# Optimization experiments

Measured on AMD Instinct MI355X. Metric: run time of the kernel, lower is better.

The kernel has to match this reference:

```python
import jax, jax.numpy as jnp
import numpy as np

B, M, T, N = 128, 256, 512, 512

def setup_inputs() -> dict:
    key = jax.random.key(0)
    ks = jax.random.split(key, 6)
    return {
        "hidden_state": jax.random.normal(ks[0], (B, M), jnp.float32),
        "cell_state": jax.random.normal(ks[1], (B, M), jnp.float32),
        "X": jax.random.normal(ks[2], (B, T, N), jnp.float32),
        "We1": jax.random.normal(ks[3], (2 * M, T), jnp.float32) * 0.05,
        "be1": jnp.zeros((T,), jnp.float32),
        "We2": jax.random.normal(ks[4], (T, T), jnp.float32) * 0.05,
        "be2": jnp.zeros((T,), jnp.float32),
        "v": jax.random.normal(ks[5], (T, 1), jnp.float32) * 0.05,
        "bv": jnp.zeros((1,), jnp.float32),
    }

def reference(hidden_state, cell_state, X, We1, be1, We2, be2, v, bv):
    # concat hidden + cell: [B, 2m]; Dense(T) then broadcast over n (K.repeat)
    hc = jnp.concatenate([hidden_state, cell_state], axis=-1)
    hs = (hc @ We1 + be1)[:, None, :]                 # [B, 1, T] (broadcast over n)
    # Permute X -> [B, n, T], Dense(T): contract over T
    ux = jnp.einsum('btn,tk->bnk', X, We2) + be2      # [B, n, T]
    # add + tanh + Dense(1) fused chain
    e = jnp.tanh(hs + ux) @ v + bv                    # [B, n, 1]
    # Permute -> [B, 1, n], softmax over last axis (n)
    attn = jax.nn.softmax(jnp.swapaxes(e, 1, 2), axis=-1)  # [B, 1, n]
    return attn
```

## Files before the change

kernel.cpp:

```cpp
#include <hip/hip_runtime.h>
#include <hip/hip_bf16.h>


typedef _Float16 half8 __attribute__((ext_vector_type(8)));
typedef float floatx4 __attribute__((ext_vector_type(4)));

__device__ __forceinline__ float fast_tanh(float x) {
    float cx = fminf(15.0f, fmaxf(-15.0f, x));
    float e = __expf(2.0f * cx);
    return (e - 1.0f) * __fdividef(1.0f, e + 1.0f);
}

__global__ __launch_bounds__(256) void k_prep_b(const float* __restrict__ We2,
                                                _Float16* __restrict__ Bf) {
    __shared__ float tl[64][133];
    const int kblk = blockIdx.x >> 3, ts = blockIdx.x & 7;
    const int k0 = kblk << 7, t0 = ts << 6;
    for (int idx = threadIdx.x; idx < 64 * 128; idx += 256) {
        int tr = idx >> 7, kc = idx & 127;
        tl[tr][kc] = We2[(t0 + tr) * 512 + k0 + kc];
    }
    __syncthreads();
    _Float16* dst = Bf + (size_t)(kblk * 8 + ts) * 8192;
#pragma unroll
    for (int i = 0; i < 4; ++i) {
        int s  = threadIdx.x + (i << 8);
        int h  = s >> 9, c = (s >> 6) & 7, ln = s & 63;
        int kl = c * 16 + (ln & 15);
        int tb = h * 32 + (ln >> 4) * 8;
        half8 hh;
#pragma unroll
        for (int j = 0; j < 8; ++j) hh[j] = (_Float16)tl[tb + j][kl];
        *(half8*)&dst[s * 8] = hh;
    }
}

__global__ __launch_bounds__(256) void k_hs(const float* __restrict__ hidden,
                                            const float* __restrict__ cell,
                                            const float* __restrict__ We1,
                                            const float* __restrict__ be1,
                                            const float* __restrict__ be2,
                                            float* __restrict__ g) {
    __shared__ __align__(16) float hcl[8][512];
    __shared__ float red[4][8][64];
    const int b0 = (blockIdx.x >> 3) << 3;
    const int k0 = (blockIdx.x & 7) << 6;
    for (int idx = threadIdx.x; idx < 8 * 512; idx += 256) {
        int bi = idx >> 9, j = idx & 511;
        hcl[bi][j] = (j < 256) ? hidden[(b0 + bi) * 256 + j]
                               : cell[(b0 + bi) * 256 + j - 256];
    }
    __syncthreads();
    const int kl = threadIdx.x & 63;
    const int jc = threadIdx.x >> 6;
    const int k  = k0 + kl;
    float acc[8] = {};
    for (int j = jc * 128; j < jc * 128 + 128; j += 4) {
        float w0 = We1[(j + 0) * 512 + k];
        float w1 = We1[(j + 1) * 512 + k];
        float w2 = We1[(j + 2) * 512 + k];
        float w3 = We1[(j + 3) * 512 + k];
#pragma unroll
        for (int bi = 0; bi < 8; ++bi) {
            float4 h = *(const float4*)&hcl[bi][j];
            acc[bi] += h.x * w0 + h.y * w1 + h.z * w2 + h.w * w3;
        }
    }
#pragma unroll
    for (int bi = 0; bi < 8; ++bi) red[jc][bi][kl] = acc[bi];
    __syncthreads();
    for (int idx = threadIdx.x; idx < 512; idx += 256) {
        int bi = idx >> 6, kk = idx & 63;
        float s = red[0][bi][kk] + red[1][bi][kk] + red[2][bi][kk] + red[3][bi][kk];
        int kg = k0 + kk;
        g[(b0 + bi) * 512 + kg] = s + be1[kg] + be2[kg];
    }
}

__global__ __launch_bounds__(256, 3) void k_main(const float* __restrict__ X,
                                                 const _Float16* __restrict__ Bf,
                                                 const float* __restrict__ g,
                                                 const float* __restrict__ vvec,
                                                 float* __restrict__ Ep) {
    __shared__ __align__(16) _Float16 Xs[2][8192];
    const int tid  = threadIdx.x;
    const int lane = tid & 63;
    const int wv   = tid >> 6;
    const int l16  = lane & 15;
    const int lhi  = lane >> 4;
    const int logical = ((blockIdx.x & 7) << 8) | (blockIdx.x >> 3);
    const int mt   = logical >> 2;
    const int kblk = logical & 3;
    const int b    = mt >> 2;
    const int n0   = (mt & 3) << 7;
    const int mw   = wv >> 1;
    const int kw   = wv & 1;

    const float* Xg = X + (size_t)b * 262144 + n0;
    int sm[4], st[4], su[4];
#pragma unroll
    for (int i = 0; i < 4; ++i) {
        int s  = tid + (i << 8);
        int m  = s & 127, lh = (s >> 7) & 3, h = s >> 9;
        sm[i] = m;
        st[i] = h * 32 + lh * 8;
        su[i] = ((h * 8 + (m >> 4)) * 64 + lh * 16 + (m & 15)) * 8;
    }
    const _Float16* Bw = Bf + (size_t)kblk * 65536 + (size_t)kw * 2048 +
                         (size_t)lane * 8;

    float xr[32];
#pragma unroll
    for (int i = 0; i < 4; ++i)
#pragma unroll
        for (int j = 0; j < 8; ++j)
            xr[i * 8 + j] = Xg[(size_t)(st[i] + j) * 512 + sm[i]];
#pragma unroll
    for (int i = 0; i < 4; ++i) {
        half8 hh;
#pragma unroll
        for (int j = 0; j < 8; ++j) hh[j] = (_Float16)xr[i * 8 + j];
        *(half8*)&Xs[0][su[i]] = hh;
    }
    __syncthreads();

    floatx4 acc[4][4];
#pragma unroll
    for (int a = 0; a < 4; ++a)
#pragma unroll
        for (int c = 0; c < 4; ++c) acc[a][c] = (floatx4){0.f, 0.f, 0.f, 0.f};

#pragma unroll
    for (int ts = 0; ts < 8; ++ts) {
        const int cur = ts & 1, nxt = cur ^ 1;
        if (ts < 7) {
#pragma unroll
            for (int i = 0; i < 4; ++i)
#pragma unroll
                for (int j = 0; j < 8; ++j)
                    xr[i * 8 + j] =
                        Xg[(size_t)((ts + 1) * 64 + st[i] + j) * 512 + sm[i]];
        }
        __builtin_amdgcn_sched_barrier(0);
#pragma unroll
        for (int h = 0; h < 2; ++h) {
            half8 af[4], bf[4];
#pragma unroll
            for (int mf = 0; mf < 4; ++mf)
                af[mf] = *(const half8*)
                    &Xs[cur][((h * 8 + mw * 4 + mf) * 64 + lane) * 8];
#pragma unroll
            for (int nf = 0; nf < 4; ++nf)
                bf[nf] = *(const half8*)
                    (Bw + (size_t)ts * 8192 + h * 4096 + nf * 512);
#pragma unroll
            for (int mf = 0; mf < 4; ++mf)
#pragma unroll
                for (int nf = 0; nf < 4; ++nf)
                    acc[mf][nf] = __builtin_amdgcn_mfma_f32_16x16x32_f16(
                        af[mf], bf[nf], acc[mf][nf], 0, 0, 0);
        }
        if (ts < 7) {
#pragma unroll
            for (int i = 0; i < 4; ++i) {
                half8 hh;
#pragma unroll
                for (int j = 0; j < 8; ++j) hh[j] = (_Float16)xr[i * 8 + j];
                *(half8*)&Xs[nxt][su[i]] = hh;
            }
        }
        __syncthreads();
    }

    const float* gb = g + b * 512 + kblk * 128;
    const float* vb = vvec + kblk * 128;
    float sl[4][4];
#pragma unroll
    for (int mf = 0; mf < 4; ++mf)
#pragma unroll
        for (int r = 0; r < 4; ++r) sl[mf][r] = 0.f;
#pragma unroll
    for (int nf = 0; nf < 4; ++nf) {
        const int kl = kw * 64 + nf * 16 + l16;
        const float gv = gb[kl];
        const float vvl = vb[kl];
#pragma unroll
        for (int mf = 0; mf < 4; ++mf)
#pragma unroll
            for (int r = 0; r < 4; ++r)
                sl[mf][r] += fast_tanh(acc[mf][nf][r] + gv) * vvl;
    }
#pragma unroll
    for (int mf = 0; mf < 4; ++mf)
#pragma unroll
        for (int r = 0; r < 4; ++r) {
            float x = sl[mf][r];
            x += __shfl_xor(x, 1);
            x += __shfl_xor(x, 2);
            x += __shfl_xor(x, 4);
            x += __shfl_xor(x, 8);
            sl[mf][r] = x;
        }
    __syncthreads();
    float* ered = (float*)&Xs[0][0];
    if (l16 == 0) {
#pragma unroll
        for (int mf = 0; mf < 4; ++mf)
#pragma unroll
            for (int r = 0; r < 4; ++r)
                ered[kw * 128 + mw * 64 + mf * 16 + lhi * 4 + r] = sl[mf][r];
    }
    __syncthreads();
    if (tid < 128) {
        float e = ered[tid] + ered[128 + tid];
        Ep[(size_t)kblk * 65536 + b * 512 + n0 + tid] = e;
    }
}

__global__ __launch_bounds__(256) void k_softmax(const float* __restrict__ Ep,
                                                 float* __restrict__ out) {
    __shared__ float rmax[4], rsum[4];
    const int b = blockIdx.x;
    const int tid = threadIdx.x;
    float e0 = Ep[b * 512 + tid] + Ep[65536 + b * 512 + tid] +
               Ep[131072 + b * 512 + tid] + Ep[196608 + b * 512 + tid];
    float e1 = Ep[b * 512 + 256 + tid] + Ep[65536 + b * 512 + 256 + tid] +
               Ep[131072 + b * 512 + 256 + tid] + Ep[196608 + b * 512 + 256 + tid];
    float m = fmaxf(e0, e1);
    for (int o = 32; o > 0; o >>= 1) m = fmaxf(m, __shfl_xor(m, o));
    if ((tid & 63) == 0) rmax[tid >> 6] = m;
    __syncthreads();
    m = fmaxf(fmaxf(rmax[0], rmax[1]), fmaxf(rmax[2], rmax[3]));
    float p0 = __expf(e0 - m), p1 = __expf(e1 - m);
    float ss = p0 + p1;
    for (int o = 32; o > 0; o >>= 1) ss += __shfl_xor(ss, o);
    if ((tid & 63) == 0) rsum[tid >> 6] = ss;
    __syncthreads();
    ss = rsum[0] + rsum[1] + rsum[2] + rsum[3];
    float inv = __fdividef(1.0f, ss);
    out[b * 512 + tid] = p0 * inv;
    out[b * 512 + 256 + tid] = p1 * inv;
}

extern "C" void kernel_launch(void* const* d_in, const int* in_sizes, int n_in,
                              void* d_out, int out_size, void* d_ws, size_t ws_size,
                              hipStream_t stream) {
    const float* hidden = (const float*)d_in[0];
    const float* cell   = (const float*)d_in[1];
    const float* X      = (const float*)d_in[2];
    const float* We1    = (const float*)d_in[3];
    const float* be1    = (const float*)d_in[4];
    const float* We2    = (const float*)d_in[5];
    const float* be2    = (const float*)d_in[6];
    const float* v      = (const float*)d_in[7];
    float* out = (float*)d_out;

    char* ws = (char*)d_ws;
    _Float16* Bf = (_Float16*)ws;
    float* g     = (float*)(ws + 524288);
    float* Ep    = (float*)(ws + 786432);

    k_prep_b<<<32, 256, 0, stream>>>(We2, Bf);
    k_hs<<<128, 256, 0, stream>>>(hidden, cell, We1, be1, be2, g);
    k_main<<<2048, 256, 0, stream>>>(X, Bf, g, v, Ep);
    k_softmax<<<128, 256, 0, stream>>>(Ep, out);
}
```

Measured before the change: 81.53 us.

## Stream X and B tiles into LDS via async global_load_lds triple buffering

The main GEMM kernel now copies fp32 X tiles and pre-packed fp16 B tiles straight into shared memory with global_load_lds DMA. It uses a three-stage ring buffer with 32-row t-slices, vmcnt waits and raw barriers in place of register staging with __syncthreads. The f32-to-f16 conversion of X moves to the LDS read side, with an XOR-swizzled layout to avoid bank conflicts, and MFMA sections get raised wave priority. The B prep kernel is repacked into 16 smaller slices per k-block to match. LDS use roughly triples, so the occupancy hint drops from 3 to 2 blocks per CU, and the scalar per-element LDS reads for A add instruction cost.

```diff
diff --git a/kernel.cpp b/kernel.cpp
--- a/kernel.cpp
+++ b/kernel.cpp
@@ -4,6 +4,10 @@
 
 typedef _Float16 half8 __attribute__((ext_vector_type(8)));
 typedef float floatx4 __attribute__((ext_vector_type(4)));
+
+#define GLOAD_LDS16(gp, lp) __builtin_amdgcn_global_load_lds(                  \
+    (const __attribute__((address_space(1))) void*)(const void*)(gp),          \
+    (__attribute__((address_space(3))) void*)(void*)(lp), 16, 0, 0)
 
 __device__ __forceinline__ float fast_tanh(float x) {
     float cx = fminf(15.0f, fmaxf(-15.0f, x));
@@ -13,25 +17,23 @@
 
 __global__ __launch_bounds__(256) void k_prep_b(const float* __restrict__ We2,
                                                 _Float16* __restrict__ Bf) {
-    __shared__ float tl[64][133];
-    const int kblk = blockIdx.x >> 3, ts = blockIdx.x & 7;
-    const int k0 = kblk << 7, t0 = ts << 6;
-    for (int idx = threadIdx.x; idx < 64 * 128; idx += 256) {
+    __shared__ float w2[32][133];
+    const int kblk = blockIdx.x >> 4, ts = blockIdx.x & 15;
+    for (int idx = threadIdx.x; idx < 32 * 128; idx += 256) {
         int tr = idx >> 7, kc = idx & 127;
-        tl[tr][kc] = We2[(t0 + tr) * 512 + k0 + kc];
-    }
-    __syncthreads();
-    _Float16* dst = Bf + (size_t)(kblk * 8 + ts) * 8192;
-#pragma unroll
-    for (int i = 0; i < 4; ++i) {
-        int s  = threadIdx.x + (i << 8);
-        int h  = s >> 9, c = (s >> 6) & 7, ln = s & 63;
-        int kl = c * 16 + (ln & 15);
-        int tb = h * 32 + (ln >> 4) * 8;
-        half8 hh;
-#pragma unroll
-        for (int j = 0; j < 8; ++j) hh[j] = (_Float16)tl[tb + j][kl];
-        *(half8*)&dst[s * 8] = hh;
+        w2[tr][kc] = We2[(ts * 32 + tr) * 512 + kblk * 128 + kc];
+    }
+    __syncthreads();
+    _Float16* dst = Bf + (size_t)blockIdx.x * 4096;
+#pragma unroll
+    for (int i = 0; i < 2; ++i) {
+        int u = threadIdx.x + (i << 8);
+        int c8 = u >> 6, l = u & 63;
+        int tl = (l >> 4) * 8, kl = c8 * 16 + (l & 15);
+        half8 h;
+#pragma unroll
+        for (int j = 0; j < 8; ++j) h[j] = (_Float16)w2[tl + j][kl];
+        *(half8*)&dst[u * 8] = h;
     }
 }
 
@@ -77,12 +79,13 @@
     }
 }
 
-__global__ __launch_bounds__(256, 3) void k_main(const float* __restrict__ X,
+__global__ __launch_bounds__(256, 2) void k_main(const float* __restrict__ X,
                                                  const _Float16* __restrict__ Bf,
                                                  const float* __restrict__ g,
                                                  const float* __restrict__ vvec,
                                                  float* __restrict__ Ep) {
-    __shared__ __align__(16) _Float16 Xs[2][8192];
+    __shared__ __align__(16) float    Xs[3][4096];
+    __shared__ __align__(16) _Float16 Bs[3][4096];
     const int tid  = threadIdx.x;
     const int lane = tid & 63;
     const int wv   = tid >> 6;
@@ -97,32 +100,36 @@
     const int kw   = wv & 1;
 
     const float* Xg = X + (size_t)b * 262144 + n0;
-    int sm[4], st[4], su[4];
-#pragma unroll
-    for (int i = 0; i < 4; ++i) {
-        int s  = tid + (i << 8);
-        int m  = s & 127, lh = (s >> 7) & 3, h = s >> 9;
-        sm[i] = m;
-        st[i] = h * 32 + lh * 8;
-        su[i] = ((h * 8 + (m >> 4)) * 64 + lh * 16 + (m & 15)) * 8;
-    }
-    const _Float16* Bw = Bf + (size_t)kblk * 65536 + (size_t)kw * 2048 +
-                         (size_t)lane * 8;
-
-    float xr[32];
-#pragma unroll
-    for (int i = 0; i < 4; ++i)
-#pragma unroll
-        for (int j = 0; j < 8; ++j)
-            xr[i * 8 + j] = Xg[(size_t)(st[i] + j) * 512 + sm[i]];
-#pragma unroll
-    for (int i = 0; i < 4; ++i) {
-        half8 hh;
-#pragma unroll
-        for (int j = 0; j < 8; ++j) hh[j] = (_Float16)xr[i * 8 + j];
-        *(half8*)&Xs[0][su[i]] = hh;
-    }
-    __syncthreads();
+    const _Float16* Bg = Bf + (size_t)kblk * 65536;
+
+    int xt[4], xcg[4];
+#pragma unroll
+    for (int p = 0; p < 4; ++p) {
+        int t = wv * 8 + p * 2 + (lane >> 5);
+        xt[p]  = t;
+        xcg[p] = (lane & 31) ^ (2 * ((t >> 3) & 3));
+    }
+    const int q = l16 >> 2, r = l16 & 3;
+    int xoff[4];
+#pragma unroll
+    for (int mf = 0; mf < 4; ++mf) {
+        int c = mw * 16 + mf * 4 + q;
+        xoff[mf] = lhi * 1024 + ((c ^ (2 * lhi)) << 2) + r;
+    }
+
+#define XDMA(ts_, bf_)                                                         \
+    { _Pragma("unroll")                                                        \
+      for (int p = 0; p < 4; ++p)                                              \
+          GLOAD_LDS16(Xg + (size_t)((ts_) * 32 + xt[p]) * 512 + xcg[p] * 4,    \
+                      &Xs[bf_][(wv * 8 + p * 2) * 128 + lane * 4]); }
+#define BDMA(ts_, bf_)                                                         \
+    { _Pragma("unroll")                                                        \
+      for (int qq = 0; qq < 2; ++qq)                                           \
+          GLOAD_LDS16(Bg + (size_t)(ts_) * 4096 + ((wv * 2 + qq) * 64 + lane) * 8, \
+                      &Bs[bf_][((wv * 2 + qq) * 64 + lane) * 8]); }
+
+    XDMA(0, 0); BDMA(0, 0);
+    XDMA(1, 1); BDMA(1, 1);
 
     floatx4 acc[4][4];
 #pragma unroll
@@ -131,45 +138,35 @@
         for (int c = 0; c < 4; ++c) acc[a][c] = (floatx4){0.f, 0.f, 0.f, 0.f};
 
 #pragma unroll
-    for (int ts = 0; ts < 8; ++ts) {
-        const int cur = ts & 1, nxt = cur ^ 1;
-        if (ts < 7) {
-#pragma unroll
-            for (int i = 0; i < 4; ++i)
-#pragma unroll
-                for (int j = 0; j < 8; ++j)
-                    xr[i * 8 + j] =
-                        Xg[(size_t)((ts + 1) * 64 + st[i] + j) * 512 + sm[i]];
+    for (int ts = 0; ts < 16; ++ts) {
+        const int bf = ts % 3;
+        if (ts < 15) asm volatile("s_waitcnt vmcnt(6)" ::: "memory");
+        else         asm volatile("s_waitcnt vmcnt(0)" ::: "memory");
+        __builtin_amdgcn_sched_barrier(0);
+        __builtin_amdgcn_s_barrier();
+        __builtin_amdgcn_sched_barrier(0);
+        half8 af[4], bfr[4];
+#pragma unroll
+        for (int mf = 0; mf < 4; ++mf)
+#pragma unroll
+            for (int j = 0; j < 8; ++j)
+                af[mf][j] = (_Float16)Xs[bf][xoff[mf] + j * 128];
+#pragma unroll
+        for (int nf = 0; nf < 4; ++nf)
+            bfr[nf] = *(const half8*)&Bs[bf][((kw * 4 + nf) * 64 + lane) * 8];
+        if (ts < 14) {
+            XDMA(ts + 2, (ts + 2) % 3);
+            BDMA(ts + 2, (ts + 2) % 3);
         }
         __builtin_amdgcn_sched_barrier(0);
-#pragma unroll
-        for (int h = 0; h < 2; ++h) {
-            half8 af[4], bf[4];
-#pragma unroll
-            for (int mf = 0; mf < 4; ++mf)
-                af[mf] = *(const half8*)
-                    &Xs[cur][((h * 8 + mw * 4 + mf) * 64 + lane) * 8];
+        __builtin_amdgcn_s_setprio(1);
+#pragma unroll
+        for (int mf = 0; mf < 4; ++mf)
 #pragma unroll
             for (int nf = 0; nf < 4; ++nf)
-                bf[nf] = *(const half8*)
-                    (Bw + (size_t)ts * 8192 + h * 4096 + nf * 512);
-#pragma unroll
-            for (int mf = 0; mf < 4; ++mf)
-#pragma unroll
-                for (int nf = 0; nf < 4; ++nf)
-                    acc[mf][nf] = __builtin_amdgcn_mfma_f32_16x16x32_f16(
-                        af[mf], bf[nf], acc[mf][nf], 0, 0, 0);
-        }
-        if (ts < 7) {
-#pragma unroll
-            for (int i = 0; i < 4; ++i) {
-                half8 hh;
-#pragma unroll
-                for (int j = 0; j < 8; ++j) hh[j] = (_Float16)xr[i * 8 + j];
-                *(half8*)&Xs[nxt][su[i]] = hh;
-            }
-        }
-        __syncthreads();
+                acc[mf][nf] = __builtin_amdgcn_mfma_f32_16x16x32_f16(
+                    af[mf], bfr[nf], acc[mf][nf], 0, 0, 0);
+        __builtin_amdgcn_s_setprio(0);
     }
 
     const float* gb = g + b * 512 + kblk * 128;
@@ -178,28 +175,28 @@
 #pragma unroll
     for (int mf = 0; mf < 4; ++mf)
 #pragma unroll
-        for (int r = 0; r < 4; ++r) sl[mf][r] = 0.f;
+        for (int rr = 0; rr < 4; ++rr) sl[mf][rr] = 0.f;
 #pragma unroll
     for (int nf = 0; nf < 4; ++nf) {
-        const int kl = kw * 64 + nf * 16 + l16;
-        const float gv = gb[kl];
-        const float vvl = vb[kl];
-#pragma unroll
-        for (int mf = 0; mf < 4; ++mf)
-#pragma unroll
-            for (int r = 0; r < 4; ++r)
-                sl[mf][r] += fast_tanh(acc[mf][nf][r] + gv) * vvl;
+        const int klc = kw * 64 + nf * 16 + l16;
+        const float gv  = gb[klc];
+        const float vvl = vb[klc];
+#pragma unroll
+        for (int mf = 0; mf < 4; ++mf)
+#pragma unroll
+            for (int rr = 0; rr < 4; ++rr)
+                sl[mf][rr] += fast_tanh(acc[mf][nf][rr] + gv) * vvl;
     }
 #pragma unroll
     for (int mf = 0; mf < 4; ++mf)
 #pragma unroll
-        for (int r = 0; r < 4; ++r) {
-            float x = sl[mf][r];
+        for (int rr = 0; rr < 4; ++rr) {
+            float x = sl[mf][rr];
             x += __shfl_xor(x, 1);
             x += __shfl_xor(x, 2);
             x += __shfl_xor(x, 4);
             x += __shfl_xor(x, 8);
-            sl[mf][r] = x;
+            sl[mf][rr] = x;
         }
     __syncthreads();
     float* ered = (float*)&Xs[0][0];
@@ -207,14 +204,16 @@
 #pragma unroll
         for (int mf = 0; mf < 4; ++mf)
 #pragma unroll
-            for (int r = 0; r < 4; ++r)
-                ered[kw * 128 + mw * 64 + mf * 16 + lhi * 4 + r] = sl[mf][r];
+            for (int rr = 0; rr < 4; ++rr)
+                ered[kw * 128 + mw * 64 + mf * 16 + lhi * 4 + rr] = sl[mf][rr];
     }
     __syncthreads();
     if (tid < 128) {
         float e = ered[tid] + ered[128 + tid];
         Ep[(size_t)kblk * 65536 + b * 512 + n0 + tid] = e;
     }
+#undef XDMA
+#undef BDMA
 }
 
 __global__ __launch_bounds__(256) void k_softmax(const float* __restrict__ Ep,
@@ -260,7 +259,7 @@
     float* g     = (float*)(ws + 524288);
     float* Ep    = (float*)(ws + 786432);
 
-    k_prep_b<<<32, 256, 0, stream>>>(We2, Bf);
+    k_prep_b<<<64, 256, 0, stream>>>(We2, Bf);
     k_hs<<<128, 256, 0, stream>>>(hidden, cell, We1, be1, be2, g);
     k_main<<<2048, 256, 0, stream>>>(X, Bf, g, v, Ep);
     k_softmax<<<128, 256, 0, stream>>>(Ep, out);
```

Result: slower. 93.69 us (+14.9%).
